# Kernel tuning notes

Hardware: AMD Instinct MI355X
Metric: run time of the kernel (lower is better)

## Reference

```python
import jax, jax.numpy as jnp
import numpy as np

N_EMBD = 1024
NUM_HEADS = 16
HEAD_SIZE = 64
B, T, T_ENC = 2, 2048, 2048


def setup_inputs() -> dict:
    key = jax.random.key(0)
    k1, k2, k3, k4, k5 = jax.random.split(key, 5)
    scale = 1.0 / np.sqrt(N_EMBD)
    return {
        "x_enc": jax.random.normal(k1, (B, T_ENC, N_EMBD), dtype=jnp.float32),
        "x": jax.random.normal(k2, (B, T, N_EMBD), dtype=jnp.float32),
        "Wk": jax.random.normal(k3, (N_EMBD, NUM_HEADS * HEAD_SIZE), dtype=jnp.float32) * scale,
        "Wq": jax.random.normal(k4, (N_EMBD, NUM_HEADS * HEAD_SIZE), dtype=jnp.float32) * scale,
        "Wv": jax.random.normal(k5, (N_EMBD, NUM_HEADS * HEAD_SIZE), dtype=jnp.float32) * scale,
    }


def reference(x_enc, x, Wk, Wq, Wv):
    b, t, c = x.shape
    _, t_enc, _ = x_enc.shape
    # projections (bias-free linears)
    k = (x_enc @ Wk).reshape(b, t_enc, NUM_HEADS, HEAD_SIZE)  # [B,S,H,D]
    v = (x_enc @ Wv).reshape(b, t_enc, NUM_HEADS, HEAD_SIZE)
    q = (x @ Wq).reshape(b, t, NUM_HEADS, HEAD_SIZE)          # [B,T,H,D]
    # NOTE: original scales by C**-0.5 with C = n_embd (not head_size)
    scale = jnp.asarray(c, x.dtype) ** -0.5
    wei = jnp.einsum("bthd,bshd->bhts", q, k) * scale          # [B,H,T,S]
    wei = jax.nn.softmax(wei, axis=-1)
    out = jnp.einsum("bhts,bshd->bthd", wei, v)                # [B,T,H,D]
    return out
```

## Files before the change

### kernel.cpp

```cpp
#include <hip/hip_runtime.h>
#include <hip/hip_bf16.h>
#include <stdint.h>

#define NE 1024
#define NH 16
#define HD 64
#define BB 2
#define TT 2048
#define MM (BB*TT)

typedef __attribute__((ext_vector_type(8))) short short8;
typedef __attribute__((ext_vector_type(4))) float floatx4;

__device__ __forceinline__ short f2bf(float f) {
    union { float f; uint32_t u; } v; v.f = f;
    uint32_t u = v.u;
    return (short)((u + 0x7fffu + ((u >> 16) & 1u)) >> 16);
}

__device__ __forceinline__ float fast_exp2(float x) {
#if __has_builtin(__builtin_amdgcn_exp2f)
    return __builtin_amdgcn_exp2f(x);
#else
    float r; asm("v_exp_f32 %0, %1" : "=v"(r) : "v"(x)); return r;
#endif
}

__device__ __forceinline__ void gload_lds16(const void* g, void* l) {
    __builtin_amdgcn_global_load_lds((__attribute__((address_space(1))) void*)g,
                                     (__attribute__((address_space(3))) void*)l,
                                     16, 0, 0);
}

__global__ void cvt_bf16_2(const float* __restrict__ ina, const float* __restrict__ inb,
                           short* __restrict__ outa, short* __restrict__ outb, int n8half) {
    int i = blockIdx.x * blockDim.x + threadIdx.x;
    const float* in; short* out; int j;
    if (i < n8half) { in = ina; out = outa; j = i; }
    else            { in = inb; out = outb; j = i - n8half; }
    const floatx4* p = (const floatx4*)(in + (size_t)j * 8);
    floatx4 a = p[0], b = p[1];
    union { uint32_t u[4]; short8 s; } r;
    asm("v_cvt_pk_bf16_f32 %0, %1, %2" : "=v"(r.u[0]) : "v"(a[0]), "v"(a[1]));
    asm("v_cvt_pk_bf16_f32 %0, %1, %2" : "=v"(r.u[1]) : "v"(a[2]), "v"(a[3]));
    asm("v_cvt_pk_bf16_f32 %0, %1, %2" : "=v"(r.u[2]) : "v"(b[0]), "v"(b[1]));
    asm("v_cvt_pk_bf16_f32 %0, %1, %2" : "=v"(r.u[3]) : "v"(b[2]), "v"(b[3]));
    *(short8*)(out + (size_t)j * 8) = r.s;
}

__global__ void wtrans(const float* __restrict__ Wq, const float* __restrict__ Wk,
                       const float* __restrict__ Wv, short* __restrict__ Wt) {
    __shared__ float t[32][33];
    const float* W = blockIdx.z == 0 ? Wq : (blockIdx.z == 1 ? Wk : Wv);
    const float sc = (blockIdx.z == 0) ? 0.04508422f : 1.0f;
    short* dst = Wt + (size_t)blockIdx.z * NE * NE;
    int n0 = blockIdx.x * 32, k0 = blockIdx.y * 32;
    int tx = threadIdx.x & 31, ty = threadIdx.x >> 5;
    #pragma unroll
    for (int i = 0; i < 4; i++)
        t[ty * 4 + i][tx] = W[(size_t)(k0 + ty * 4 + i) * NE + n0 + tx];
    __syncthreads();
    #pragma unroll
    for (int i = 0; i < 4; i++)
        dst[(size_t)(n0 + ty * 4 + i) * NE + k0 + tx] = f2bf(t[tx][ty * 4 + i] * sc);
}

__global__ void __launch_bounds__(256) gemm_bt(const short* __restrict__ x_bf,
                                               const short* __restrict__ xenc_bf,
                                               const short* __restrict__ Wt,
                                               short* __restrict__ qkv) {
    __shared__ short sA[3][4096];
    __shared__ short sB[3][4096];
    const int bid = blockIdx.x;
    const int xcd = bid & 7, inner = bid >> 3;
    const int xblk = inner & 7;
    const int yh = (inner >> 3) & 3;
    const int z = inner >> 5;
    const int yblk = xcd + 8 * yh;

    const short* A  = (z == 0) ? x_bf : xenc_bf;
    const short* Bt = Wt + (size_t)z * NE * NE;
    short* C = qkv + (size_t)z * MM * NE;

    const int tid = threadIdx.x;
    const int lane = tid & 63, wid = tid >> 6;
    const int l15 = lane & 15, lg = lane >> 4;
    const int wr = wid >> 1, wc = wid & 1;
    const int m0 = yblk * 128, n0 = xblk * 128;

    const short* gA = A  + (size_t)(m0 + (tid >> 2)) * NE + (tid & 3) * 8;
    const short* gB = Bt + (size_t)(n0 + (tid >> 2)) * NE + (tid & 3) * 8;

    floatx4 acc[4][4];
    floatx4 zero = {0.f, 0.f, 0.f, 0.f};
    #pragma unroll
    for (int i = 0; i < 4; i++)
        #pragma unroll
        for (int j = 0; j < 4; j++) acc[i][j] = zero;

#define GSTAGE(bi, kt) do { \
    gload_lds16(gA + (kt),            &sA[bi][wid * 512]); \
    gload_lds16(gA + 64 * NE + (kt),  &sA[bi][wid * 512 + 2048]); \
    gload_lds16(gB + (kt),            &sB[bi][wid * 512]); \
    gload_lds16(gB + 64 * NE + (kt),  &sB[bi][wid * 512 + 2048]); \
} while (0)

#define GCOMP(cur) do { \
    short8 af[4], bfr[4]; \
    _Pragma("unroll") \
    for (int i = 0; i < 4; i++) { \
        af[i]  = *(const short8*)&sA[cur][(wr * 64 + i * 16 + l15) * 32 + lg * 8]; \
        bfr[i] = *(const short8*)&sB[cur][(wc * 64 + i * 16 + l15) * 32 + lg * 8]; \
    } \
    __builtin_amdgcn_s_setprio(1); \
    _Pragma("unroll") \
    for (int i = 0; i < 4; i++) \
        _Pragma("unroll") \
        for (int j = 0; j < 4; j++) \
            acc[i][j] = __builtin_amdgcn_mfma_f32_16x16x32_bf16(af[i], bfr[j], acc[i][j], 0, 0, 0); \
    __builtin_amdgcn_s_setprio(0); \
} while (0)

    GSTAGE(0, 0);
    GSTAGE(1, 32);
    for (int t = 0; t < 31; ++t) {
        asm volatile("s_waitcnt vmcnt(4)" ::: "memory");
        __builtin_amdgcn_sched_barrier(0);
        __builtin_amdgcn_s_barrier();
        __builtin_amdgcn_sched_barrier(0);
        if (t < 30) GSTAGE((t + 2) % 3, (t + 2) * 32);
        GCOMP(t % 3);
    }
    asm volatile("s_waitcnt vmcnt(0)" ::: "memory");
    __builtin_amdgcn_sched_barrier(0);
    __builtin_amdgcn_s_barrier();
    __builtin_amdgcn_sched_barrier(0);
    GCOMP(1);
#undef GSTAGE
#undef GCOMP

    #pragma unroll
    for (int i = 0; i < 4; i++)
        #pragma unroll
        for (int j = 0; j < 4; j++)
            #pragma unroll
            for (int r = 0; r < 4; r++) {
                int row = m0 + wr * 64 + i * 16 + lg * 4 + r;
                int col = n0 + wc * 64 + j * 16 + l15;
                C[(size_t)row * NE + col] = f2bf(acc[i][j][r]);
            }
}

__global__ void vtrans(const short* __restrict__ v, short* __restrict__ vt) {
    __shared__ short t[64][65];
    int s0 = blockIdx.x * 64;
    int bh = blockIdx.y;
    int b = bh >> 4, h = bh & 15;
    int tid = threadIdx.x;
    int c = tid & 63, rr = tid >> 6;
    #pragma unroll
    for (int i = 0; i < 16; i++)
        t[i * 4 + rr][c] = v[(size_t)(b * TT + s0 + i * 4 + rr) * NE + h * HD + c];
    __syncthreads();
    int csw = (c & 35) | (((c >> 4) & 1) << 2) | (((c >> 2) & 3) << 3);
    #pragma unroll
    for (int i = 0; i < 16; i++)
        vt[(size_t)(bh * HD + i * 4 + rr) * TT + s0 + csw] = t[c][i * 4 + rr];
}

__global__ void __launch_bounds__(256, 2) fattn(const short* __restrict__ q,
                                                const short* __restrict__ k,
                                                const short* __restrict__ vt,
                                                float* __restrict__ out) {
    __shared__ short kbuf[3][4096];
    __shared__ short vbuf[3][4096];
    const int tid = threadIdx.x, lane = tid & 63, wid = tid >> 6;
    const int l15 = lane & 15, lg = lane >> 4;
    const int bid = blockIdx.x;
    const int xcd = bid & 7, rest = bid >> 3;
    const int qblk = rest & 15;
    const int bh = xcd + 8 * (rest >> 4);
    const int b = bh >> 4, h = bh & 15;
    const int q0 = qblk * 128 + wid * 32;

    short8 qf[2][2];
    #pragma unroll
    for (int qb = 0; qb < 2; qb++) {
        const short* qp = q + (size_t)(b * TT + q0 + qb * 16 + l15) * NE + h * HD + lg * 8;
        qf[qb][0] = *(const short8*)qp;
        qf[qb][1] = *(const short8*)(qp + 32);
    }
    short8 ones;
    #pragma unroll
    for (int j = 0; j < 8; j++) ones[j] = (short)0x3F80;

    floatx4 acc_o[2][4];
    floatx4 acc_l[2];
    floatx4 zero = {0.f, 0.f, 0.f, 0.f};
    floatx4 minus8 = {-8.f, -8.f, -8.f, -8.f};
    #pragma unroll
    for (int qb = 0; qb < 2; qb++) {
        acc_l[qb] = zero;
        #pragma unroll
        for (int db = 0; db < 4; db++) acc_o[qb][db] = zero;
    }

    const char* kgb = (const char*)(k + (size_t)(b * TT) * NE + h * HD);
    const char* vgb = (const char*)(vt + (size_t)bh * HD * TT);
    const int srow = tid >> 3;
    const int ssw  = ((tid & 7) * 16) ^ ((srow & 7) << 4);
    const char* ksrc = kgb + (size_t)srow * (NE * 2) + ssw;
    const char* vsrc = vgb + (size_t)srow * (TT * 2) + ssw;

    const int swz  = (l15 & 7) << 4;
    const int rd0  = l15 * 128 + ((lg * 16) ^ swz);
    const int rd1  = l15 * 128 + ((64 + lg * 16) ^ swz);

#define STAGE(bi, s0v) do { \
    const char* ks_ = ksrc + (size_t)(s0v) * (NE * 2); \
    gload_lds16(ks_,                 &kbuf[bi][wid * 512]); \
    gload_lds16(ks_ + 32 * (NE * 2), &kbuf[bi][wid * 512 + 2048]); \
    const char* vs_ = vsrc + (size_t)(s0v) * 2; \
    gload_lds16(vs_,                 &vbuf[bi][wid * 512]); \
    gload_lds16(vs_ + 32 * (TT * 2), &vbuf[bi][wid * 512 + 2048]); \
} while (0)

#define KREAD(bi) do { \
    const char* kb_ = (const char*)kbuf[bi]; \
    _Pragma("unroll") \
    for (int cb = 0; cb < 4; cb++) { \
        kfr[cb][0] = *(const short8*)(kb_ + cb * 2048 + rd0); \
        kfr[cb][1] = *(const short8*)(kb_ + cb * 2048 + rd1); \
    } \
} while (0)

#define VREAD(bi) do { \
    const char* vb_ = (const char*)vbuf[bi]; \
    _Pragma("unroll") \
    for (int db = 0; db < 4; db++) { \
        vf[0][db] = *(const short8*)(vb_ + db * 2048 + rd0); \
        vf[1][db] = *(const short8*)(vb_ + db * 2048 + rd1); \
    } \
} while (0)

#define QK() do { \
    _Pragma("unroll") \
    for (int qb = 0; qb < 2; qb++) \
        _Pragma("unroll") \
        for (int cb = 0; cb < 4; cb++) sacc[qb][cb] = minus8; \
    __builtin_amdgcn_s_setprio(1); \
    _Pragma("unroll") \
    for (int qb = 0; qb < 2; qb++) \
        _Pragma("unroll") \
        for (int cb = 0; cb < 4; cb++) { \
            sacc[qb][cb] = __builtin_amdgcn_mfma_f32_16x16x32_bf16(kfr[cb][0], qf[qb][0], sacc[qb][cb], 0, 0, 0); \
            sacc[qb][cb] = __builtin_amdgcn_mfma_f32_16x16x32_bf16(kfr[cb][1], qf[qb][1], sacc[qb][cb], 0, 0, 0); \
        } \
    __builtin_amdgcn_s_setprio(0); \
} while (0)

#define EXPCVT() do { \
    _Pragma("unroll") \
    for (int qb = 0; qb < 2; qb++) { \
        float pe[16]; \
        _Pragma("unroll") \
        for (int cb = 0; cb < 4; cb++) \
            _Pragma("unroll") \
            for (int r = 0; r < 4; r++) \
                pe[cb * 4 + r] = fast_exp2(sacc[qb][cb][r]); \
        _Pragma("unroll") \
        for (int ks = 0; ks < 2; ks++) { \
            union { uint32_t u[4]; short8 s; } pk_; \
            _Pragma("unroll") \
            for (int j2 = 0; j2 < 4; j2++) \
                asm("v_cvt_pk_bf16_f32 %0, %1, %2" \
                    : "=v"(pk_.u[j2]) \
                    : "v"(pe[ks * 8 + 2 * j2]), "v"(pe[ks * 8 + 2 * j2 + 1])); \
            paf[qb][ks] = pk_.s; \
        } \
    } \
} while (0)

#define PVH(qb) do { \
    __builtin_amdgcn_s_setprio(1); \
    _Pragma("unroll") \
    for (int ks = 0; ks < 2; ks++) { \
        _Pragma("unroll") \
        for (int db = 0; db < 4; db++) \
            acc_o[qb][db] = __builtin_amdgcn_mfma_f32_16x16x32_bf16(paf[qb][ks], vf[ks][db], acc_o[qb][db], 0, 0, 0); \
        acc_l[qb] = __builtin_amdgcn_mfma_f32_16x16x32_bf16(paf[qb][ks], ones, acc_l[qb], 0, 0, 0); \
    } \
    __builtin_amdgcn_s_setprio(0); \
} while (0)

    short8 kfr[4][2];
    short8 vf[2][4];
    short8 paf[2][2];
    floatx4 sacc[2][4];

    STAGE(0, 0);
    STAGE(1, 64);
    STAGE(2, 128);
    asm volatile("s_waitcnt vmcnt(0)" ::: "memory");
    __builtin_amdgcn_sched_barrier(0);
    __builtin_amdgcn_s_barrier();
    __builtin_amdgcn_sched_barrier(0);
    KREAD(0);
    VREAD(0);
    QK();
    EXPCVT();

    for (int t = 0; t < 31; ++t) {
        KREAD((t + 1) % 3);
        PVH(0);
        QK();
        PVH(1);
        VREAD((t + 1) % 3);
        EXPCVT();
        asm volatile("s_waitcnt vmcnt(0)" ::: "memory");
        __builtin_amdgcn_sched_barrier(0);
        __builtin_amdgcn_s_barrier();
        __builtin_amdgcn_sched_barrier(0);
        if (t <= 28) STAGE(t % 3, (t + 3) * 64);
    }
    PVH(0);
    PVH(1);
#undef STAGE
#undef KREAD
#undef VREAD
#undef QK
#undef EXPCVT
#undef PVH

    #pragma unroll
    for (int qb = 0; qb < 2; qb++) {
        #pragma unroll
        for (int r = 0; r < 4; r++) {
            float inv = 1.0f / acc_l[qb][r];
            #pragma unroll
            for (int db = 0; db < 4; db++)
                out[(size_t)(b * TT + q0 + qb * 16 + lg * 4 + r) * NE + h * HD + db * 16 + l15] =
                    acc_o[qb][db][r] * inv;
        }
    }
}

extern "C" void kernel_launch(void* const* d_in, const int* in_sizes, int n_in,
                              void* d_out, int out_size, void* d_ws, size_t ws_size,
                              hipStream_t stream) {
    const float* x_enc = (const float*)d_in[0];
    const float* x     = (const float*)d_in[1];
    const float* Wk    = (const float*)d_in[2];
    const float* Wq    = (const float*)d_in[3];
    const float* Wv    = (const float*)d_in[4];
    float* out = (float*)d_out;

    const size_t SZ = (size_t)MM * NE;
    short* x_bf    = (short*)d_ws;
    short* xenc_bf = x_bf + SZ;
    short* Wt      = xenc_bf + SZ;
    short* qkv     = Wt + 3 * (size_t)NE * NE;
    short* vt      = qkv + 3 * SZ;

    cvt_bf16_2<<<dim3(4096), dim3(256), 0, stream>>>(x, x_enc, x_bf, xenc_bf, (int)(SZ / 8));
    wtrans<<<dim3(32, 32, 3), dim3(256), 0, stream>>>(Wq, Wk, Wv, Wt);
    gemm_bt<<<dim3(768), dim3(256), 0, stream>>>(x_bf, xenc_bf, Wt, qkv);
    vtrans<<<dim3(32, 32), dim3(256), 0, stream>>>(qkv + 2 * SZ, vt);
    fattn<<<dim3(512), dim3(256), 0, stream>>>(qkv, qkv + SZ, vt, out);
}
```

Measured before the change: 89.69 us.

## Double query rows per attention wave to reuse K/V fragments and interleave softmax

Each wave now handles 64 query rows (four 16-row blocks) instead of 32, so every K/V tile loaded into LDS and registers serves twice as many queries. The grid shrinks from 512 to 256 blocks and launch bounds drop to one block per SIMD to make room for the larger accumulator state. The loop is restructured into two halves whose QK, exp and PV phases are interleaved so MFMA work overlaps the exp/convert work of the other half. The risk is lower occupancy and fewer blocks than CUs (256 on a 256-CU part), so latency hiding relies entirely on the in-wave interleave.

```diff
diff --git a/kernel.cpp b/kernel.cpp
--- a/kernel.cpp
+++ b/kernel.cpp
@@ -168,7 +168,7 @@
         vt[(size_t)(bh * HD + i * 4 + rr) * TT + s0 + csw] = t[c][i * 4 + rr];
 }
 
-__global__ void __launch_bounds__(256, 2) fattn(const short* __restrict__ q,
+__global__ void __launch_bounds__(256, 1) fattn(const short* __restrict__ q,
                                                 const short* __restrict__ k,
                                                 const short* __restrict__ vt,
                                                 float* __restrict__ out) {
@@ -178,14 +178,14 @@
     const int l15 = lane & 15, lg = lane >> 4;
     const int bid = blockIdx.x;
     const int xcd = bid & 7, rest = bid >> 3;
-    const int qblk = rest & 15;
-    const int bh = xcd + 8 * (rest >> 4);
+    const int qblk = rest & 7;
+    const int bh = xcd + 8 * (rest >> 3);
     const int b = bh >> 4, h = bh & 15;
-    const int q0 = qblk * 128 + wid * 32;
-
-    short8 qf[2][2];
-    #pragma unroll
-    for (int qb = 0; qb < 2; qb++) {
+    const int q0 = qblk * 256 + wid * 64;
+
+    short8 qf[4][2];
+    #pragma unroll
+    for (int qb = 0; qb < 4; qb++) {
         const short* qp = q + (size_t)(b * TT + q0 + qb * 16 + l15) * NE + h * HD + lg * 8;
         qf[qb][0] = *(const short8*)qp;
         qf[qb][1] = *(const short8*)(qp + 32);
@@ -194,12 +194,12 @@
     #pragma unroll
     for (int j = 0; j < 8; j++) ones[j] = (short)0x3F80;
 
-    floatx4 acc_o[2][4];
-    floatx4 acc_l[2];
+    floatx4 acc_o[4][4];
+    floatx4 acc_l[4];
     floatx4 zero = {0.f, 0.f, 0.f, 0.f};
     floatx4 minus8 = {-8.f, -8.f, -8.f, -8.f};
     #pragma unroll
-    for (int qb = 0; qb < 2; qb++) {
+    for (int qb = 0; qb < 4; qb++) {
         acc_l[qb] = zero;
         #pragma unroll
         for (int db = 0; db < 4; db++) acc_o[qb][db] = zero;
@@ -243,31 +243,31 @@
     } \
 } while (0)
 
-#define QK() do { \
-    _Pragma("unroll") \
-    for (int qb = 0; qb < 2; qb++) \
-        _Pragma("unroll") \
-        for (int cb = 0; cb < 4; cb++) sacc[qb][cb] = minus8; \
+#define QK2(base) do { \
+    _Pragma("unroll") \
+    for (int q2 = 0; q2 < 2; q2++) \
+        _Pragma("unroll") \
+        for (int cb = 0; cb < 4; cb++) sacc[q2][cb] = minus8; \
     __builtin_amdgcn_s_setprio(1); \
     _Pragma("unroll") \
-    for (int qb = 0; qb < 2; qb++) \
+    for (int q2 = 0; q2 < 2; q2++) \
         _Pragma("unroll") \
         for (int cb = 0; cb < 4; cb++) { \
-            sacc[qb][cb] = __builtin_amdgcn_mfma_f32_16x16x32_bf16(kfr[cb][0], qf[qb][0], sacc[qb][cb], 0, 0, 0); \
-            sacc[qb][cb] = __builtin_amdgcn_mfma_f32_16x16x32_bf16(kfr[cb][1], qf[qb][1], sacc[qb][cb], 0, 0, 0); \
+            sacc[q2][cb] = __builtin_amdgcn_mfma_f32_16x16x32_bf16(kfr[cb][0], qf[(base) + q2][0], sacc[q2][cb], 0, 0, 0); \
+            sacc[q2][cb] = __builtin_amdgcn_mfma_f32_16x16x32_bf16(kfr[cb][1], qf[(base) + q2][1], sacc[q2][cb], 0, 0, 0); \
         } \
     __builtin_amdgcn_s_setprio(0); \
 } while (0)
 
-#define EXPCVT() do { \
-    _Pragma("unroll") \
-    for (int qb = 0; qb < 2; qb++) { \
+#define EXP2(PAF) do { \
+    _Pragma("unroll") \
+    for (int q2 = 0; q2 < 2; q2++) { \
         float pe[16]; \
         _Pragma("unroll") \
         for (int cb = 0; cb < 4; cb++) \
             _Pragma("unroll") \
             for (int r = 0; r < 4; r++) \
-                pe[cb * 4 + r] = fast_exp2(sacc[qb][cb][r]); \
+                pe[cb * 4 + r] = fast_exp2(sacc[q2][cb][r]); \
         _Pragma("unroll") \
         for (int ks = 0; ks < 2; ks++) { \
             union { uint32_t u[4]; short8 s; } pk_; \
@@ -276,26 +276,26 @@
                 asm("v_cvt_pk_bf16_f32 %0, %1, %2" \
                     : "=v"(pk_.u[j2]) \
                     : "v"(pe[ks * 8 + 2 * j2]), "v"(pe[ks * 8 + 2 * j2 + 1])); \
-            paf[qb][ks] = pk_.s; \
+            PAF[q2][ks] = pk_.s; \
         } \
     } \
 } while (0)
 
-#define PVH(qb) do { \
+#define PV1(qb_, PAFQ) do { \
     __builtin_amdgcn_s_setprio(1); \
     _Pragma("unroll") \
     for (int ks = 0; ks < 2; ks++) { \
         _Pragma("unroll") \
         for (int db = 0; db < 4; db++) \
-            acc_o[qb][db] = __builtin_amdgcn_mfma_f32_16x16x32_bf16(paf[qb][ks], vf[ks][db], acc_o[qb][db], 0, 0, 0); \
-        acc_l[qb] = __builtin_amdgcn_mfma_f32_16x16x32_bf16(paf[qb][ks], ones, acc_l[qb], 0, 0, 0); \
+            acc_o[qb_][db] = __builtin_amdgcn_mfma_f32_16x16x32_bf16(PAFQ[ks], vf[ks][db], acc_o[qb_][db], 0, 0, 0); \
+        acc_l[qb_] = __builtin_amdgcn_mfma_f32_16x16x32_bf16(PAFQ[ks], ones, acc_l[qb_], 0, 0, 0); \
     } \
     __builtin_amdgcn_s_setprio(0); \
 } while (0)
 
     short8 kfr[4][2];
     short8 vf[2][4];
-    short8 paf[2][2];
+    short8 pafA[2][2], pafB[2][2];
     floatx4 sacc[2][4];
 
     STAGE(0, 0);
@@ -307,33 +307,41 @@
     __builtin_amdgcn_sched_barrier(0);
     KREAD(0);
     VREAD(0);
-    QK();
-    EXPCVT();
+    QK2(0);
+    EXP2(pafA);
+    QK2(2);
+    EXP2(pafB);
 
     for (int t = 0; t < 31; ++t) {
         KREAD((t + 1) % 3);
-        PVH(0);
-        QK();
-        PVH(1);
+        PV1(0, pafA[0]);
+        QK2(0);
+        PV1(1, pafA[1]);
+        EXP2(pafA);
+        PV1(2, pafB[0]);
+        QK2(2);
+        PV1(3, pafB[1]);
         VREAD((t + 1) % 3);
-        EXPCVT();
+        EXP2(pafB);
         asm volatile("s_waitcnt vmcnt(0)" ::: "memory");
         __builtin_amdgcn_sched_barrier(0);
         __builtin_amdgcn_s_barrier();
         __builtin_amdgcn_sched_barrier(0);
         if (t <= 28) STAGE(t % 3, (t + 3) * 64);
     }
-    PVH(0);
-    PVH(1);
+    PV1(0, pafA[0]);
+    PV1(1, pafA[1]);
+    PV1(2, pafB[0]);
+    PV1(3, pafB[1]);
 #undef STAGE
 #undef KREAD
 #undef VREAD
-#undef QK
-#undef EXPCVT
-#undef PVH
-
-    #pragma unroll
-    for (int qb = 0; qb < 2; qb++) {
+#undef QK2
+#undef EXP2
+#undef PV1
+
+    #pragma unroll
+    for (int qb = 0; qb < 4; qb++) {
         #pragma unroll
         for (int r = 0; r < 4; r++) {
             float inv = 1.0f / acc_l[qb][r];
@@ -366,5 +374,5 @@
     wtrans<<<dim3(32, 32, 3), dim3(256), 0, stream>>>(Wq, Wk, Wv, Wt);
     gemm_bt<<<dim3(768), dim3(256), 0, stream>>>(x_bf, xenc_bf, Wt, qkv);
     vtrans<<<dim3(32, 32), dim3(256), 0, stream>>>(qkv + 2 * SZ, vt);
-    fattn<<<dim3(512), dim3(256), 0, stream>>>(qkv, qkv + SZ, vt, out);
-}
+    fattn<<<dim3(256), dim3(256), 0, stream>>>(qkv, qkv + SZ, vt, out);
+}
```

After: 104.5 us. +16.6%, slower.
